# Kernel optimization log

Hardware: AMD Instinct MI355X
Metric: run time of the kernel (lower is better)

The kernel has to match this reference:

```python
import jax, jax.numpy as jnp
import numpy as np

B, N, DIM = 4, 2048, 512
H, DH = 8, 64  # n_heads, dim_head; inner = H*DH = 512
SCALE = DH ** -0.5


def setup_inputs() -> dict:
    key = jax.random.key(0)
    k1, k2, k3 = jax.random.split(key, 3)
    inner = H * DH
    X = jax.random.normal(k1, (B, N, DIM), dtype=jnp.float32)
    W_qkv = jax.random.normal(k2, (DIM, 3 * inner), dtype=jnp.float32) * (DIM ** -0.5)
    W_out = jax.random.normal(k3, (inner, DIM), dtype=jnp.float32) * (inner ** -0.5)
    b_out = jnp.zeros((DIM,), dtype=jnp.float32)
    return {"X": X, "W_qkv": W_qkv, "W_out": W_out, "b_out": b_out}


def reference(X, W_qkv, W_out, b_out):
    # X: (b, n, dim)
    qkv = X @ W_qkv                      # (b, n, 3*h*d)
    q, k, v = jnp.split(qkv, 3, axis=-1)
    def to_heads(t):
        b, n, _ = t.shape
        return t.reshape(b, n, H, DH).transpose(0, 2, 1, 3)  # (b, h, n, d)
    q, k, v = to_heads(q), to_heads(k), to_heads(v)
    # NOTE: original computes scores[n, m] = k_n . q_m and softmaxes over m (query axis)
    scores = jnp.einsum('bhnd,bhmd->bhnm', k, q) * SCALE     # (b, h, n_k, m_q)
    att = jax.nn.softmax(scores, axis=-1)
    # out token axis is the KEY index n: out[n, d] = sum_e att[n, e] * v[e, d]
    out = jnp.einsum('bhne,bhed->bhnd', att, v)              # (b, h, n, d)
    out = out.transpose(0, 2, 1, 3).reshape(X.shape[0], X.shape[1], H * DH)  # (b, n, h*d)
    return out @ W_out + b_out
```

## Files before the change

kernel.cpp:

```cpp
#include <hip/hip_runtime.h>
#include <hip/hip_bf16.h>

typedef __bf16 bf16_t;
typedef bf16_t bf16x8 __attribute__((ext_vector_type(8)));
typedef bf16_t bf16x4v __attribute__((ext_vector_type(4)));
typedef float f32x4 __attribute__((ext_vector_type(4)));
typedef float f32x16 __attribute__((ext_vector_type(16)));
typedef int i32x4 __attribute__((ext_vector_type(4)));

#define B_SZ 4
#define N_TOK 2048
#define DIM 512
#define H_N 8
#define DH 64
#define INNER 512
#define M_ROWS 8192
#define NQKV 1536
#define K_FOLD 0.18033688011112042f

#define GLD_LDS16(gp, lp)                                          \
  __builtin_amdgcn_global_load_lds(                                \
      (const __attribute__((address_space(1))) void*)(gp),         \
      (__attribute__((address_space(3))) void*)(lp), 16, 0, 0)

__device__ __forceinline__ float fexp2(float x) {
#if __has_builtin(__builtin_amdgcn_exp2f)
  return __builtin_amdgcn_exp2f(x);
#else
  float r;
  asm volatile("v_exp_f32 %0, %1\n\ts_nop 1" : "=v"(r) : "v"(x));
  return r;
#endif
}

__device__ __forceinline__ int cvtpk_bf16(float lo, float hi) {
  int r;
  asm("v_cvt_pk_bf16_f32 %0, %1, %2" : "=v"(r) : "v"(lo), "v"(hi));
  return r;
}

__device__ __forceinline__ void permswap32(int& a, int& b) {
  asm volatile("v_permlane32_swap_b32 %0, %1" : "+v"(a), "+v"(b));
}


__global__ void f32_to_bf16_kernel(const float* __restrict__ src,
                                   bf16_t* __restrict__ dst, int n4) {
  int i = blockIdx.x * blockDim.x + threadIdx.x;
  int stride = gridDim.x * blockDim.x;
  for (; i < n4; i += stride) {
    float4 f = reinterpret_cast<const float4*>(src)[i];
    bf16x4v o;
    o.x = (bf16_t)f.x; o.y = (bf16_t)f.y; o.z = (bf16_t)f.z; o.w = (bf16_t)f.w;
    reinterpret_cast<bf16x4v*>(dst)[i] = o;
  }
}

__global__ void transpose_f32_to_bf16_kernel(const float* __restrict__ src,
                                             bf16_t* __restrict__ dst, int R, int C) {
  int t = blockIdx.x * blockDim.x + threadIdx.x;
  if (t >= R * C) return;
  int r = t / C, c = t - r * C;
  dst[(size_t)c * R + r] = (bf16_t)src[t];
}

template <int MODE>
__global__ __launch_bounds__(256) void gemm_bf16_kernel(
    const bf16_t* __restrict__ A, const bf16_t* __restrict__ Bt,
    int M, int Nn, int K,
    bf16_t* __restrict__ qb, bf16_t* __restrict__ kb, bf16_t* __restrict__ vtb,
    float* __restrict__ outF, const float* __restrict__ bias) {
  __shared__ bf16_t As[128 * 64];
  __shared__ bf16_t Bs[128 * 64];

  const int tid = threadIdx.x;
  const int lane = tid & 63;
  const int wave = tid >> 6;
  const int g = lane >> 4, c = lane & 15;
  const int wm = (wave >> 1) * 64, wn = (wave & 1) * 64;
  const int m0 = blockIdx.x * 128, n0 = blockIdx.y * 128;

  f32x4 acc[4][4] = {};

  for (int k0 = 0; k0 < K; k0 += 64) {
    __syncthreads();
    #pragma unroll
    for (int i = 0; i < 4; ++i) {
      int blk = i * 256 + tid;
      int row = blk >> 3;
      int cb = (blk & 7) ^ (row & 7);
      int base = (i * 256 + wave * 64) * 8;
      GLD_LDS16(A + (size_t)(m0 + row) * K + k0 + cb * 8, &As[base]);
      GLD_LDS16(Bt + (size_t)(n0 + row) * K + k0 + cb * 8, &Bs[base]);
    }
    __syncthreads();
    __builtin_amdgcn_s_setprio(1);
    #pragma unroll
    for (int ks = 0; ks < 2; ++ks) {
      bf16x8 af[4], bfr[4];
      #pragma unroll
      for (int i = 0; i < 4; ++i) {
        af[i] = *reinterpret_cast<const bf16x8*>(
            &As[(wm + i * 16 + c) * 64 + (((ks * 4 + g) ^ (c & 7)) * 8)]);
        bfr[i] = *reinterpret_cast<const bf16x8*>(
            &Bs[(wn + i * 16 + c) * 64 + (((ks * 4 + g) ^ (c & 7)) * 8)]);
      }
      #pragma unroll
      for (int mi = 0; mi < 4; ++mi)
        #pragma unroll
        for (int ni = 0; ni < 4; ++ni)
          acc[mi][ni] = __builtin_amdgcn_mfma_f32_16x16x32_bf16(
              af[mi], bfr[ni], acc[mi][ni], 0, 0, 0);
    }
    __builtin_amdgcn_s_setprio(0);
  }

  #pragma unroll
  for (int mi = 0; mi < 4; ++mi) {
    #pragma unroll
    for (int ni = 0; ni < 4; ++ni) {
      int colg = n0 + wn + ni * 16 + c;
      if (MODE == 0) {
        int s = colg >> 9;
        int hh = (colg >> 6) & 7, dd = colg & 63;
        int rowg0 = m0 + wm + mi * 16 + g * 4;
        int bb = rowg0 >> 11, nn = rowg0 & 2047;
        if (s == 2) {
          bf16x4v pk;
          pk.x = (bf16_t)acc[mi][ni][0];
          pk.y = (bf16_t)acc[mi][ni][1];
          pk.z = (bf16_t)acc[mi][ni][2];
          pk.w = (bf16_t)acc[mi][ni][3];
          *reinterpret_cast<bf16x4v*>(
              &vtb[(((size_t)(bb * H_N + hh)) * DH + dd) * N_TOK + nn]) = pk;
        } else {
          float sc = (s == 1) ? K_FOLD : 1.0f;
          bf16_t* dst = (s == 0) ? qb : kb;
          #pragma unroll
          for (int r = 0; r < 4; ++r)
            dst[(((size_t)(bb * H_N + hh)) * N_TOK + nn + r) * DH + dd] =
                (bf16_t)(acc[mi][ni][r] * sc);
        }
      } else {
        #pragma unroll
        for (int r = 0; r < 4; ++r) {
          int rowg = m0 + wm + mi * 16 + g * 4 + r;
          outF[(size_t)rowg * Nn + colg] = acc[mi][ni][r] + bias[colg];
        }
      }
    }
  }
}

__global__ __launch_bounds__(512, 4) void attn_kernel(
    const bf16_t* __restrict__ Qproj, const bf16_t* __restrict__ Kproj,
    const bf16_t* __restrict__ Vt, bf16_t* __restrict__ att_out) {
  const int glin = blockIdx.x;
  const int xcd = glin & 7;
  const int jj = glin >> 3;
  const int hb = xcd * 4 + (jj >> 4);
  const int rb = jj & 15;
  const int h = hb & 7, b = hb >> 3;

  const size_t hbo = (size_t)(b * H_N + h);
  const bf16_t* Aq = Kproj + hbo * N_TOK * DH;
  const bf16_t* Ak = Qproj + hbo * N_TOK * DH;
  const bf16_t* Av = Vt + hbo * (size_t)(DH * N_TOK);

  const int tid = threadIdx.x, lane = tid & 63, wave = tid >> 6;
  const int nl = lane & 31;
  const int hf = lane >> 5;
  const int grp = wave >> 2;
  const int gw = wave & 3;
  const int r0 = rb * 128, wr0 = gw * 32;
  const int kv0 = grp * 1024;

  __shared__ __align__(16) char smem[65536];
  bf16_t* sKg = (bf16_t*)(smem + grp * 32768);
  bf16_t* sVg = (bf16_t*)(smem + grp * 32768 + 16384);

  bf16x8 qreg[4];
  #pragma unroll
  for (int ks = 0; ks < 4; ++ks)
    qreg[ks] = *reinterpret_cast<const bf16x8*>(
        &Aq[(size_t)(r0 + wr0 + nl) * DH + ks * 16 + hf * 8]);

  f32x16 accO0 = {}, accO1 = {};
  float Lp[4] = {};

  const int gtid = tid & 255;
  auto stage = [&](int buf, int j0) {
    #pragma unroll
    for (int i = 0; i < 2; ++i) {
      int idx = i * 256 + gtid;
      int row = idx >> 3;
      int cb = (idx & 7) ^ (row & 7);
      int base = buf * 4096 + (i * 256 + gw * 64) * 8;
      GLD_LDS16(Ak + (size_t)(j0 + row) * DH + cb * 8, sKg + base);
      GLD_LDS16(Av + (size_t)row * N_TOK + j0 + cb * 8, sVg + base);
    }
  };

  stage(0, kv0);
  __syncthreads();

  constexpr int NT = 16;
  for (int t = 0; t < NT; ++t) {
    if (t + 1 < NT) stage((t + 1) & 1, kv0 + (t + 1) * 64);
    const bf16_t* bK = sKg + (t & 1) * 4096;
    const bf16_t* bV = sVg + (t & 1) * 4096;

    f32x16 aT[2] = {};
    __builtin_amdgcn_s_setprio(1);
    #pragma unroll
    for (int ks = 0; ks < 4; ++ks) {
      #pragma unroll
      for (int mi = 0; mi < 2; ++mi) {
        int rowt = mi * 32 + nl;
        bf16x8 ak = *reinterpret_cast<const bf16x8*>(
            &bK[rowt * 64 + (((ks * 2 + hf) ^ (rowt & 7)) * 8)]);
        aT[mi] = __builtin_amdgcn_mfma_f32_32x32x16_bf16(
            ak, qreg[ks], aT[mi], 0, 0, 0);
      }
    }
    __builtin_amdgcn_s_setprio(0);

    #pragma unroll
    for (int r = 0; r < 16; ++r) {
      float p0 = fexp2(aT[0][r]); aT[0][r] = p0;
      float p1 = fexp2(aT[1][r]); aT[1][r] = p1;
      Lp[r & 3] += p0 + p1;
    }

    i32x4 pk[4];
    #pragma unroll
    for (int ks = 0; ks < 4; ++ks) {
      const int mi = ks >> 1, base = (ks & 1) * 8;
      int a0 = cvtpk_bf16(aT[mi][base + 0], aT[mi][base + 1]);
      int b0 = cvtpk_bf16(aT[mi][base + 4], aT[mi][base + 5]);
      int a1 = cvtpk_bf16(aT[mi][base + 2], aT[mi][base + 3]);
      int b1 = cvtpk_bf16(aT[mi][base + 6], aT[mi][base + 7]);
      permswap32(a0, b0);
      permswap32(a1, b1);
      pk[ks].x = a0; pk[ks].y = a1; pk[ks].z = b0; pk[ks].w = b1;
    }

    __builtin_amdgcn_s_setprio(1);
    #pragma unroll
    for (int ks = 0; ks < 4; ++ks) {
      bf16x8 pfrag = __builtin_bit_cast(bf16x8, pk[ks]);
      int rv0 = nl, rv1 = 32 + nl;
      bf16x8 av0 = *reinterpret_cast<const bf16x8*>(
          &bV[rv0 * 64 + (((ks * 2 + hf) ^ (rv0 & 7)) * 8)]);
      bf16x8 av1 = *reinterpret_cast<const bf16x8*>(
          &bV[rv1 * 64 + (((ks * 2 + hf) ^ (rv1 & 7)) * 8)]);
      accO0 = __builtin_amdgcn_mfma_f32_32x32x16_bf16(av0, pfrag, accO0, 0, 0, 0);
      accO1 = __builtin_amdgcn_mfma_f32_32x32x16_bf16(av1, pfrag, accO1, 0, 0, 0);
    }
    __builtin_amdgcn_s_setprio(0);

    __syncthreads();
  }

  float Lsum = (Lp[0] + Lp[1]) + (Lp[2] + Lp[3]);
  float* mb = (float*)smem;
  const int moff = (gw * 64 + lane) * 36;
  if (grp == 1) {
    #pragma unroll
    for (int r = 0; r < 16; ++r) {
      mb[moff + r] = accO0[r];
      mb[moff + 16 + r] = accO1[r];
    }
    mb[moff + 32] = Lsum;
  }
  __syncthreads();
  if (grp == 0) {
    #pragma unroll
    for (int r = 0; r < 16; ++r) {
      accO0[r] += mb[moff + r];
      accO1[r] += mb[moff + 16 + r];
    }
    float l = Lsum + mb[moff + 32];
    l += __shfl_xor(l, 32);
    float invL = 1.0f / l;
    const int nrow = r0 + wr0 + nl;
    #pragma unroll
    for (int q = 0; q < 4; ++q) {
      int d0a = 8 * q + 4 * hf;
      bf16x4v o;
      o.x = (bf16_t)(accO0[4 * q + 0] * invL);
      o.y = (bf16_t)(accO0[4 * q + 1] * invL);
      o.z = (bf16_t)(accO0[4 * q + 2] * invL);
      o.w = (bf16_t)(accO0[4 * q + 3] * invL);
      *reinterpret_cast<bf16x4v*>(
          &att_out[((size_t)(b * N_TOK) + nrow) * INNER + h * DH + d0a]) = o;
      bf16x4v o2;
      o2.x = (bf16_t)(accO1[4 * q + 0] * invL);
      o2.y = (bf16_t)(accO1[4 * q + 1] * invL);
      o2.z = (bf16_t)(accO1[4 * q + 2] * invL);
      o2.w = (bf16_t)(accO1[4 * q + 3] * invL);
      *reinterpret_cast<bf16x4v*>(
          &att_out[((size_t)(b * N_TOK) + nrow) * INNER + h * DH + 32 + d0a]) = o2;
    }
  }
}


extern "C" void kernel_launch(void* const* d_in, const int* in_sizes, int n_in,
                              void* d_out, int out_size, void* d_ws, size_t ws_size,
                              hipStream_t stream) {
  const float* X    = (const float*)d_in[0];
  const float* Wqkv = (const float*)d_in[1];
  const float* Wout = (const float*)d_in[2];
  const float* bout = (const float*)d_in[3];
  float* out = (float*)d_out;

  char* ws = (char*)d_ws;
  bf16_t* Xb    = (bf16_t*)(ws);
  bf16_t* WqkvT = (bf16_t*)(ws + 8388608);
  bf16_t* WoutT = (bf16_t*)(ws + 9961472);
  bf16_t* Qb    = (bf16_t*)(ws + 10485760);
  bf16_t* Kb    = (bf16_t*)(ws + 18874368);
  bf16_t* Vtb   = (bf16_t*)(ws + 27262976);
  bf16_t* AttO  = (bf16_t*)(ws + 35651584);

  f32_to_bf16_kernel<<<2048, 256, 0, stream>>>(X, Xb, (M_ROWS * DIM) / 4);
  transpose_f32_to_bf16_kernel<<<(DIM * NQKV + 255) / 256, 256, 0, stream>>>(
      Wqkv, WqkvT, DIM, NQKV);
  transpose_f32_to_bf16_kernel<<<(INNER * DIM + 255) / 256, 256, 0, stream>>>(
      Wout, WoutT, INNER, DIM);

  dim3 g1(M_ROWS / 128, NQKV / 128);
  gemm_bf16_kernel<0><<<g1, 256, 0, stream>>>(Xb, WqkvT, M_ROWS, NQKV, DIM,
                                              Qb, Kb, Vtb, nullptr, nullptr);

  attn_kernel<<<dim3(512), 512, 0, stream>>>(Qb, Kb, Vtb, AttO);

  dim3 g3(M_ROWS / 128, DIM / 128);
  gemm_bf16_kernel<1><<<g3, 256, 0, stream>>>(AttO, WoutT, M_ROWS, DIM, DIM,
                                              nullptr, nullptr, nullptr, out, bout);
}
```

Measured before the change: 90.46 us.

## Pre-swizzle V into MFMA fragment layout and load it directly to registers

The QKV projection epilogue now writes V in a layout that matches the MFMA operand fragment order, so each lane reads its V fragment with contiguous 16-byte global loads. The V tiles no longer go through LDS staging, which roughly halves shared memory use and cuts LDS traffic in the attention loop. The V loads are issued at the top of each iteration, so their global latency has to be hidden behind the QK MFMAs. The merge buffer stride also changes from 36 to 37, which looks aimed at avoiding LDS bank conflicts.

```diff
diff --git a/kernel.cpp b/kernel.cpp
--- a/kernel.cpp
+++ b/kernel.cpp
@@ -131,8 +131,13 @@
           pk.y = (bf16_t)acc[mi][ni][1];
           pk.z = (bf16_t)acc[mi][ni][2];
           pk.w = (bf16_t)acc[mi][ni][3];
+          int tt = nn >> 7;
+          int chv = (nn >> 6) & 1, ksv = (nn >> 4) & 3, hfv = (nn >> 3) & 1;
+          int vi = dd >> 5, nlv = dd & 31;
           *reinterpret_cast<bf16x4v*>(
-              &vtb[(((size_t)(bb * H_N + hh)) * DH + dd) * N_TOK + nn]) = pk;
+              &vtb[(size_t)(bb * H_N + hh) * (DH * N_TOK)
+                   + tt * 8192 + (vi * 8 + chv * 4 + ksv) * 512
+                   + (hfv * 32 + nlv) * 8 + (nn & 7)]) = pk;
         } else {
           float sc = (s == 1) ? K_FOLD : 1.0f;
           bf16_t* dst = (s == 0) ? qb : kb;
@@ -175,9 +180,8 @@
   const int r0 = rb * 128, wr0 = gw * 32;
   const int kv0 = grp * 1024;
 
-  __shared__ __align__(16) char smem[65536];
-  bf16_t* sKg = (bf16_t*)(smem + grp * 32768);
-  bf16_t* sVg = (bf16_t*)(smem + grp * 32768 + 16384);
+  __shared__ __align__(16) char smem[38912];
+  bf16_t* sKg = (bf16_t*)(smem + grp * 16384);
 
   bf16x8 qreg[4];
   #pragma unroll
@@ -189,7 +193,7 @@
   float Lp[4] = {};
 
   const int gtid = tid & 255;
-  auto stage = [&](int buf, int j0) {
+  auto stageK = [&](int buf, int j0) {
     #pragma unroll
     for (int i = 0; i < 2; ++i) {
       int idx = i * 256 + gtid;
@@ -197,18 +201,26 @@
       int cb = (idx & 7) ^ (row & 7);
       int base = buf * 4096 + (i * 256 + gw * 64) * 8;
       GLD_LDS16(Ak + (size_t)(j0 + row) * DH + cb * 8, sKg + base);
-      GLD_LDS16(Av + (size_t)row * N_TOK + j0 + cb * 8, sVg + base);
     }
   };
 
-  stage(0, kv0);
+  stageK(0, kv0);
   __syncthreads();
 
   constexpr int NT = 16;
   for (int t = 0; t < NT; ++t) {
-    if (t + 1 < NT) stage((t + 1) & 1, kv0 + (t + 1) * 64);
+    const int j0 = kv0 + t * 64;
+    const int tt = j0 >> 7, ch = (j0 >> 6) & 1;
+    bf16x8 av[2][4];
+    #pragma unroll
+    for (int vi = 0; vi < 2; ++vi)
+      #pragma unroll
+      for (int ks = 0; ks < 4; ++ks)
+        av[vi][ks] = *reinterpret_cast<const bf16x8*>(
+            &Av[(size_t)tt * 8192 + (vi * 8 + ch * 4 + ks) * 512 + lane * 8]);
+
+    if (t + 1 < NT) stageK((t + 1) & 1, kv0 + (t + 1) * 64);
     const bf16_t* bK = sKg + (t & 1) * 4096;
-    const bf16_t* bV = sVg + (t & 1) * 4096;
 
     f32x16 aT[2] = {};
     __builtin_amdgcn_s_setprio(1);
@@ -232,7 +244,7 @@
       Lp[r & 3] += p0 + p1;
     }
 
-    i32x4 pk[4];
+    __builtin_amdgcn_s_setprio(1);
     #pragma unroll
     for (int ks = 0; ks < 4; ++ks) {
       const int mi = ks >> 1, base = (ks & 1) * 8;
@@ -242,20 +254,10 @@
       int b1 = cvtpk_bf16(aT[mi][base + 6], aT[mi][base + 7]);
       permswap32(a0, b0);
       permswap32(a1, b1);
-      pk[ks].x = a0; pk[ks].y = a1; pk[ks].z = b0; pk[ks].w = b1;
-    }
-
-    __builtin_amdgcn_s_setprio(1);
-    #pragma unroll
-    for (int ks = 0; ks < 4; ++ks) {
-      bf16x8 pfrag = __builtin_bit_cast(bf16x8, pk[ks]);
-      int rv0 = nl, rv1 = 32 + nl;
-      bf16x8 av0 = *reinterpret_cast<const bf16x8*>(
-          &bV[rv0 * 64 + (((ks * 2 + hf) ^ (rv0 & 7)) * 8)]);
-      bf16x8 av1 = *reinterpret_cast<const bf16x8*>(
-          &bV[rv1 * 64 + (((ks * 2 + hf) ^ (rv1 & 7)) * 8)]);
-      accO0 = __builtin_amdgcn_mfma_f32_32x32x16_bf16(av0, pfrag, accO0, 0, 0, 0);
-      accO1 = __builtin_amdgcn_mfma_f32_32x32x16_bf16(av1, pfrag, accO1, 0, 0, 0);
+      i32x4 w; w.x = a0; w.y = a1; w.z = b0; w.w = b1;
+      bf16x8 pfrag = __builtin_bit_cast(bf16x8, w);
+      accO0 = __builtin_amdgcn_mfma_f32_32x32x16_bf16(av[0][ks], pfrag, accO0, 0, 0, 0);
+      accO1 = __builtin_amdgcn_mfma_f32_32x32x16_bf16(av[1][ks], pfrag, accO1, 0, 0, 0);
     }
     __builtin_amdgcn_s_setprio(0);
 
@@ -264,7 +266,7 @@
 
   float Lsum = (Lp[0] + Lp[1]) + (Lp[2] + Lp[3]);
   float* mb = (float*)smem;
-  const int moff = (gw * 64 + lane) * 36;
+  const int moff = (gw * 64 + lane) * 37;
   if (grp == 1) {
     #pragma unroll
     for (int r = 0; r < 16; ++r) {
```

Result: slower. 100.5 us (+11.1%).
